# Kernel optimization log

Measured on AMD Instinct MI355X. Metric: run time of the kernel, lower is better.

Reference implementation:

```python
import jax, jax.numpy as jnp
import numpy as np

N1, N2, N3, N4 = 50_000, 100_000, 200_000, 400_000
D, OUT = 128, 128


def silu(x):
    return x * jax.nn.sigmoid(x)


def mlp(h, Wa, ba, Wb, bb):
    # torch.nn.Sequential(Linear, SiLU, Linear)
    return silu(h @ Wa + ba) @ Wb + bb


def setup_inputs() -> dict:
    key = jax.random.key(0)
    ks = jax.random.split(key, 12)
    s = 1.0 / np.sqrt(D).astype(np.float32)
    inp = {
        "feat": jax.random.normal(ks[0], (N1, D), jnp.float32),
        "W1a": jax.random.normal(ks[1], (D, D), jnp.float32) * s,
        "b1a": jnp.zeros((D,), jnp.float32),
        "W1b": jax.random.normal(ks[2], (D, D), jnp.float32) * s,
        "b1b": jnp.zeros((D,), jnp.float32),
        "W2a": jax.random.normal(ks[3], (D, D), jnp.float32) * s,
        "b2a": jnp.zeros((D,), jnp.float32),
        "W2b": jax.random.normal(ks[4], (D, D), jnp.float32) * s,
        "b2b": jnp.zeros((D,), jnp.float32),
        "W3a": jax.random.normal(ks[5], (D, D), jnp.float32) * s,
        "b3a": jnp.zeros((D,), jnp.float32),
        "W3b": jax.random.normal(ks[6], (D, D), jnp.float32) * s,
        "b3b": jnp.zeros((D,), jnp.float32),
        "Wo": jax.random.normal(ks[7], (3 * D, OUT), jnp.float32) * (1.0 / np.sqrt(3 * D).astype(np.float32)),
        "bo": jnp.zeros((OUT,), jnp.float32),
        # n{k-1}_in_n{k} edges: each level-k path has exactly 2 subpath children
        "src12": jax.random.randint(ks[8], (2 * N2,), 0, N1),
        "dst12": jnp.repeat(jnp.arange(N2), 2),
        "src23": jax.random.randint(ks[9], (2 * N3,), 0, N2),
        "dst23": jnp.repeat(jnp.arange(N3), 2),
        "src34": jax.random.randint(ks[10], (2 * N4,), 0, N3),
        "dst34": jnp.repeat(jnp.arange(N4), 2),
    }
    return inp


def reference(feat, W1a, b1a, W1b, b1b, W2a, b2a, W2b, b2b,
              W3a, b3a, W3b, b3b, Wo, bo,
              src12, dst12, src23, dst23, src34, dst34):
    # ---- upward ----
    h1 = mlp(feat, W1a, b1a, W1b, b1b)                       # n1 features (kept for final concat)
    h2 = jax.ops.segment_prod(h1[src12], dst12, num_segments=N2, indices_are_sorted=True)
    h2t = mlp(h2, W2a, b2a, W2b, b2b)
    h3 = jax.ops.segment_prod(h2t[src23], dst23, num_segments=N3, indices_are_sorted=True)
    h3t = mlp(h3, W3a, b3a, W3b, b3b)
    h4 = jax.ops.segment_prod(h3t[src34], dst34, num_segments=N4, indices_are_sorted=True)
    # ---- downward ----
    # n2_has_n1 (reverse of n1_in_n2): sum n2 features onto n1 -> 'h2'
    h2_on_n1 = jax.ops.segment_sum(h2t[dst12], src12, num_segments=N1)
    # n4_has_n3 then n3_has_n2 (overwrite h on lower level)
    h3_dn = jax.ops.segment_sum(h4[dst34], src34, num_segments=N3)
    h2_dn = jax.ops.segment_sum(h3_dn[dst23], src23, num_segments=N2)
    # n2_has_n1 again -> 'h_down'
    h_down = jax.ops.segment_sum(h2_dn[dst12], src12, num_segments=N1)
    # final per-node linear + SiLU on concat([h, h2, h_down])
    out = silu(jnp.concatenate([h1, h2_on_n1, h_down], axis=-1) @ Wo + bo)
    return out
```

## Files before the change

kernel.cpp:

```cpp
#include <hip/hip_runtime.h>

#define D 128
#define XSH 136

#define SHIFT 11
#define NPB   2048
#define EPT   8

typedef _Float16 f16;
typedef __attribute__((ext_vector_type(4))) _Float16 f16x4;
typedef __attribute__((ext_vector_type(8))) _Float16 f16x8;
typedef __attribute__((ext_vector_type(4))) float    f32x4;

__device__ __forceinline__ float silu_f(float x) {
    return x / (1.0f + __expf(-x));
}

struct WPtrs { const float* s0; const float* s1; const float* s2;
               const float* s3; const float* s4; const float* s5; };
__global__ void wconv_all_kernel(WPtrs wp, const float* __restrict__ Wo, f16* __restrict__ WT)
{
    const int blk = blockIdx.x, t = threadIdx.x;
    if (blk < 384) {
        const int wid = blk >> 6;
        const int off = ((blk & 63) << 8) + t;
        const int n = off >> 7, k = off & 127;
        const float* s;
        switch (wid) {
            case 0: s = wp.s0; break;
            case 1: s = wp.s1; break;
            case 2: s = wp.s2; break;
            case 3: s = wp.s3; break;
            case 4: s = wp.s4; break;
            default: s = wp.s5; break;
        }
        WT[(wid << 14) + off] = (f16)s[(k << 7) + n];
    } else {
        const int off = ((blk - 384) << 8) + t;
        const int n = off / 384, k = off - n * 384;
        WT[(6 << 14) + off] = (f16)Wo[k * 128 + n];
    }
}

template<bool GATHER>
__launch_bounds__(256)
__global__ void mlp_mfma_kernel(const void* __restrict__ in_, const int* __restrict__ src,
                                const f16* __restrict__ WaT, const float* __restrict__ ba,
                                const f16* __restrict__ WbT, const float* __restrict__ bb,
                                f16* __restrict__ out, int nrows)
{
    __shared__ f16 xs[64][XSH];
    __shared__ f16 ys[64][XSH];
    const int t = threadIdx.x;
    const int w = t >> 6, l = t & 63;
    const int cl = l & 15, kg = l >> 4;
    const int row0 = blockIdx.x * 64;

    f16x8 wa[2][4], wb[2][4];
    #pragma unroll
    for (int nt = 0; nt < 2; ++nt)
        #pragma unroll
        for (int kk = 0; kk < 4; ++kk) {
            const size_t o = (size_t)((w * 2 + nt) * 16 + cl) * D + kk * 32 + kg * 8;
            wa[nt][kk] = *(const f16x8*)(WaT + o);
            wb[nt][kk] = *(const f16x8*)(WbT + o);
        }

    {
        const int r = t >> 2, q = t & 3;
        const int g = row0 + r;
        f16* dst = &xs[r][q * 32];
        if (g < nrows) {
            if (GATHER) {
                const f16* in = (const f16*)in_;
                const int a = src[2 * g], b = src[2 * g + 1];
                const f16x8* pa = (const f16x8*)(in + (size_t)a * D + q * 32);
                const f16x8* pb = (const f16x8*)(in + (size_t)b * D + q * 32);
                #pragma unroll
                for (int i = 0; i < 4; ++i) {
                    f16x8 av = pa[i], bv = pb[i], hv;
                    #pragma unroll
                    for (int j = 0; j < 8; ++j) hv[j] = (f16)((float)av[j] * (float)bv[j]);
                    *(f16x8*)(dst + 8 * i) = hv;
                }
            } else {
                const float* in = (const float*)in_;
                const float4* p = (const float4*)(in + (size_t)g * D + q * 32);
                #pragma unroll
                for (int i = 0; i < 4; ++i) {
                    float4 v0 = p[2 * i], v1 = p[2 * i + 1];
                    f16x8 hv = {(f16)v0.x, (f16)v0.y, (f16)v0.z, (f16)v0.w,
                                (f16)v1.x, (f16)v1.y, (f16)v1.z, (f16)v1.w};
                    *(f16x8*)(dst + 8 * i) = hv;
                }
            }
        } else {
            f16x8 z = {};
            #pragma unroll
            for (int i = 0; i < 4; ++i) *(f16x8*)(dst + 8 * i) = z;
        }
    }
    __syncthreads();

    f32x4 acc[2][4];

    #pragma unroll
    for (int nt = 0; nt < 2; ++nt)
        #pragma unroll
        for (int m = 0; m < 4; ++m) acc[nt][m] = (f32x4){0.f, 0.f, 0.f, 0.f};
    #pragma unroll
    for (int m = 0; m < 4; ++m)
        #pragma unroll
        for (int kk = 0; kk < 4; ++kk) {
            const f16x8 a = *(const f16x8*)&xs[m * 16 + cl][kk * 32 + kg * 8];
            acc[0][m] = __builtin_amdgcn_mfma_f32_16x16x32_f16(wa[0][kk], a, acc[0][m], 0, 0, 0);
            acc[1][m] = __builtin_amdgcn_mfma_f32_16x16x32_f16(wa[1][kk], a, acc[1][m], 0, 0, 0);
        }
    #pragma unroll
    for (int nt = 0; nt < 2; ++nt) {
        const int n0 = w * 32 + nt * 16 + kg * 4;
        const float4 bv = *(const float4*)&ba[n0];
        #pragma unroll
        for (int m = 0; m < 4; ++m) {
            f16x4 y;
            y[0] = (f16)silu_f(acc[nt][m][0] + bv.x);
            y[1] = (f16)silu_f(acc[nt][m][1] + bv.y);
            y[2] = (f16)silu_f(acc[nt][m][2] + bv.z);
            y[3] = (f16)silu_f(acc[nt][m][3] + bv.w);
            *(f16x4*)&ys[m * 16 + cl][n0] = y;
        }
    }
    __syncthreads();

    #pragma unroll
    for (int nt = 0; nt < 2; ++nt)
        #pragma unroll
        for (int m = 0; m < 4; ++m) acc[nt][m] = (f32x4){0.f, 0.f, 0.f, 0.f};
    #pragma unroll
    for (int m = 0; m < 4; ++m)
        #pragma unroll
        for (int kk = 0; kk < 4; ++kk) {
            const f16x8 a = *(const f16x8*)&ys[m * 16 + cl][kk * 32 + kg * 8];
            acc[0][m] = __builtin_amdgcn_mfma_f32_16x16x32_f16(wb[0][kk], a, acc[0][m], 0, 0, 0);
            acc[1][m] = __builtin_amdgcn_mfma_f32_16x16x32_f16(wb[1][kk], a, acc[1][m], 0, 0, 0);
        }
    #pragma unroll
    for (int nt = 0; nt < 2; ++nt) {
        const int n0 = w * 32 + nt * 16 + kg * 4;
        const float4 bv = *(const float4*)&bb[n0];
        #pragma unroll
        for (int m = 0; m < 4; ++m) {
            f16x4 z;
            z[0] = (f16)(acc[nt][m][0] + bv.x);
            z[1] = (f16)(acc[nt][m][1] + bv.y);
            z[2] = (f16)(acc[nt][m][2] + bv.z);
            z[3] = (f16)(acc[nt][m][3] + bv.w);
            *(f16x4*)&xs[m * 16 + cl][n0] = z;
        }
    }
    __syncthreads();

    {
        const int r = t >> 2, q = t & 3;
        const int g = row0 + r;
        if (g < nrows) {
            f16* dst = out + (size_t)g * D + q * 32;
            #pragma unroll
            for (int i = 0; i < 4; ++i)
                *(f16x8*)(dst + 8 * i) = *(const f16x8*)&xs[r][q * 32 + 8 * i];
        }
    }
}

__launch_bounds__(256)
__global__ void out_mfma_kernel(const f16* __restrict__ h1, const f16* __restrict__ h2on1,
                                const f16* __restrict__ hdown,
                                const f16* __restrict__ WoT, const float* __restrict__ bo,
                                float* __restrict__ out, int nrows)
{
    __shared__ f16 xs[64][XSH];
    const int t = threadIdx.x;
    const int w = t >> 6, l = t & 63;
    const int cl = l & 15, kg = l >> 4;
    const int row0 = blockIdx.x * 64;

    f32x4 acc[2][4];
    #pragma unroll
    for (int nt = 0; nt < 2; ++nt)
        #pragma unroll
        for (int m = 0; m < 4; ++m) acc[nt][m] = (f32x4){0.f, 0.f, 0.f, 0.f};

    const f16* parts[3] = {h1, h2on1, hdown};
    #pragma unroll
    for (int p = 0; p < 3; ++p) {
        f16x8 wo[2][4];
        #pragma unroll
        for (int nt = 0; nt < 2; ++nt)
            #pragma unroll
            for (int kk = 0; kk < 4; ++kk)
                wo[nt][kk] = *(const f16x8*)(WoT + (size_t)((w * 2 + nt) * 16 + cl) * 384
                                             + p * D + kk * 32 + kg * 8);
        {
            const int r = t >> 2, q = t & 3;
            const int g = row0 + r;
            f16* dst = &xs[r][q * 32];
            if (g < nrows) {
                const f16x8* pp = (const f16x8*)(parts[p] + (size_t)g * D + q * 32);
                #pragma unroll
                for (int i = 0; i < 4; ++i) *(f16x8*)(dst + 8 * i) = pp[i];
            } else {
                f16x8 z = {};
                #pragma unroll
                for (int i = 0; i < 4; ++i) *(f16x8*)(dst + 8 * i) = z;
            }
        }
        __syncthreads();
        #pragma unroll
        for (int m = 0; m < 4; ++m)
            #pragma unroll
            for (int kk = 0; kk < 4; ++kk) {
                const f16x8 a = *(const f16x8*)&xs[m * 16 + cl][kk * 32 + kg * 8];
                acc[0][m] = __builtin_amdgcn_mfma_f32_16x16x32_f16(wo[0][kk], a, acc[0][m], 0, 0, 0);
                acc[1][m] = __builtin_amdgcn_mfma_f32_16x16x32_f16(wo[1][kk], a, acc[1][m], 0, 0, 0);
            }
        __syncthreads();
    }

    #pragma unroll
    for (int nt = 0; nt < 2; ++nt) {
        const int n0 = w * 32 + nt * 16 + kg * 4;
        const float4 bv = *(const float4*)&bo[n0];
        #pragma unroll
        for (int m = 0; m < 4; ++m) {
            const int g = row0 + m * 16 + cl;
            if (g < nrows) {
                float4 v = make_float4(silu_f(acc[nt][m][0] + bv.x),
                                       silu_f(acc[nt][m][1] + bv.y),
                                       silu_f(acc[nt][m][2] + bv.z),
                                       silu_f(acc[nt][m][3] + bv.w));
                *(float4*)(out + (size_t)g * D + n0) = v;
            }
        }
    }
}

__global__ void bucket_hist_kernel(const int* __restrict__ s12, int E12,
                                   const int* __restrict__ s23, int E23,
                                   const int* __restrict__ s34, int E34,
                                   int* __restrict__ bcnt, int N1, int N2, int nbkt)
{
    __shared__ int h[256];
    const int t = threadIdx.x;
    for (int i = t; i < 256; i += blockDim.x) h[i] = 0;
    __syncthreads();
    const int Etot = E12 + E23 + E34;
    for (int g = blockIdx.x * blockDim.x + t; g < Etot; g += gridDim.x * blockDim.x) {
        int node;
        if (g < E12) node = s12[g];
        else if (g < E12 + E23) node = N1 + s23[g - E12];
        else node = N1 + N2 + s34[g - E12 - E23];
        atomicAdd(&h[node >> SHIFT], 1);
    }
    __syncthreads();
    for (int i = t; i < nbkt; i += blockDim.x)
        if (h[i]) atomicAdd(&bcnt[i], h[i]);
}

__global__ void bucket_scan_kernel(const int* __restrict__ bcnt, int* __restrict__ bbase,
                                   int* __restrict__ bcur, int nbkt, int Etot)
{
    __shared__ int s[256];
    const int t = threadIdx.x;
    const int v = (t < nbkt) ? bcnt[t] : 0;
    s[t] = v;
    __syncthreads();
    for (int d = 1; d < 256; d <<= 1) {
        const int u = (t >= d) ? s[t - d] : 0;
        __syncthreads();
        s[t] += u;
        __syncthreads();
    }
    if (t < nbkt) { const int ex = s[t] - v; bbase[t] = ex; bcur[t] = ex; }
    if (t == 0) bbase[nbkt] = Etot;
}

__global__ void csr_pass1_kernel(const int* __restrict__ s12, int E12,
                                 const int* __restrict__ s23, int E23,
                                 const int* __restrict__ s34, int E34,
                                 int* __restrict__ bcur, int2* __restrict__ recs,
                                 int N1, int N2, int nbkt)
{
    __shared__ int cnt[256];
    __shared__ int gbase[256];
    const int t = threadIdx.x;
    const int chunk = blockIdx.x * (256 * EPT);
    const int Etot = E12 + E23 + E34;
    for (int i = t; i < 256; i += 256) cnt[i] = 0;
    __syncthreads();
    int node_[EPT], pay_[EPT], br_[EPT];
    #pragma unroll
    for (int i = 0; i < EPT; ++i) {
        const int g = chunk + i * 256 + t;
        int node = -1, pay = 0, b = 0, r = 0;
        if (g < Etot) {
            if (g < E12) { node = s12[g]; pay = g >> 1; }
            else if (g < E12 + E23) { const int e = g - E12; node = N1 + s23[e]; pay = e >> 1; }
            else { const int e = g - E12 - E23; node = N1 + N2 + s34[e]; pay = s34[e ^ 1]; }
            b = node >> SHIFT;
            r = atomicAdd(&cnt[b], 1);
        }
        node_[i] = node; pay_[i] = pay; br_[i] = (b << 16) | r;
    }
    __syncthreads();
    if (t < nbkt && cnt[t]) gbase[t] = atomicAdd(&bcur[t], cnt[t]);
    __syncthreads();
    #pragma unroll
    for (int i = 0; i < EPT; ++i) {
        if (node_[i] >= 0) {
            const int b = br_[i] >> 16, r = br_[i] & 0xffff;
            recs[gbase[b] + r] = make_int2(node_[i], pay_[i]);
        }
    }
}

__launch_bounds__(1024)
__global__ void csr_pass2_kernel(const int2* __restrict__ recs,
                                 const int* __restrict__ bbase,
                                 int2* __restrict__ offcnt, int* __restrict__ el, int NT)
{
    __shared__ int cnt2[NPB];
    __shared__ int pref[NPB];
    __shared__ int s1[NPB / 2];
    const int b = blockIdx.x, t = threadIdx.x;
    const int node0 = b << SHIFT;
    const int k0 = bbase[b], k1 = bbase[b + 1];
    for (int i = t; i < NPB; i += 1024) cnt2[i] = 0;
    __syncthreads();
    for (int k = k0 + t; k < k1; k += 1024)
        atomicAdd(&cnt2[recs[k].x - node0], 1);
    __syncthreads();
    s1[t] = cnt2[2 * t] + cnt2[2 * t + 1];
    __syncthreads();
    for (int d = 1; d < 1024; d <<= 1) {
        const int u = (t >= d) ? s1[t - d] : 0;
        __syncthreads();
        s1[t] += u;
        __syncthreads();
    }
    {
        const int a = cnt2[2 * t];
        const int pairsum = a + cnt2[2 * t + 1];
        const int ex0 = s1[t] - pairsum;
        pref[2 * t] = ex0;
        pref[2 * t + 1] = ex0 + a;
    }
    __syncthreads();
    for (int i = t; i < NPB; i += 1024) {
        const int node = node0 + i;
        if (node < NT) offcnt[node] = make_int2(k0 + pref[i], cnt2[i]);
    }
    __syncthreads();
    for (int k = k0 + t; k < k1; k += 1024) {
        const int2 r = recs[k];
        const int pos = atomicAdd(&pref[r.x - node0], 1);
        el[k0 + pos] = r.y;
    }
}

__global__ void prod_gather_kernel(const f16* __restrict__ h3t,
                                   const int2* __restrict__ offcnt,
                                   const int* __restrict__ el,
                                   f16* __restrict__ h3dn, int nrows)
{
    const long long g = (long long)blockIdx.x * blockDim.x + threadIdx.x;
    const int i = (int)(g >> 4);
    if (i >= nrows) return;
    const int c = ((int)g & 15) * 8;
    const f16x8 ownv = *(const f16x8*)(h3t + (size_t)i * D + c);
    float acc0[8] = {}, acc1[8] = {};
    const int2 oc = offcnt[i];
    const int base = oc.x, deg = oc.y;
    int d = 0;
    for (; d + 4 <= deg; d += 4) {
        const int s0 = el[base + d + 0], s1v = el[base + d + 1];
        const int s2 = el[base + d + 2], s3v = el[base + d + 3];
        const f16x8 v0 = *(const f16x8*)(h3t + (size_t)s0 * D + c);
        const f16x8 v1 = *(const f16x8*)(h3t + (size_t)s1v * D + c);
        const f16x8 v2 = *(const f16x8*)(h3t + (size_t)s2 * D + c);
        const f16x8 v3 = *(const f16x8*)(h3t + (size_t)s3v * D + c);
        #pragma unroll
        for (int j = 0; j < 8; ++j) {
            acc0[j] += (float)v0[j] + (float)v2[j];
            acc1[j] += (float)v1[j] + (float)v3[j];
        }
    }
    for (; d < deg; ++d) {
        const int s0 = el[base + d];
        const f16x8 v0 = *(const f16x8*)(h3t + (size_t)s0 * D + c);
        #pragma unroll
        for (int j = 0; j < 8; ++j) acc0[j] += (float)v0[j];
    }
    f16x8 r;
    #pragma unroll
    for (int j = 0; j < 8; ++j) r[j] = (f16)((acc0[j] + acc1[j]) * (float)ownv[j]);
    *(f16x8*)(h3dn + (size_t)i * D + c) = r;
}

__global__ void gather_sum_kernel(const f16* __restrict__ val,
                                  const int2* __restrict__ offcnt,
                                  const int* __restrict__ el,
                                  f16* __restrict__ dst, int nrows)
{
    const long long g = (long long)blockIdx.x * blockDim.x + threadIdx.x;
    const int i = (int)(g >> 4);
    if (i >= nrows) return;
    const int c = ((int)g & 15) * 8;
    float acc0[8] = {}, acc1[8] = {};
    const int2 oc = offcnt[i];
    const int base = oc.x, deg = oc.y;
    int d = 0;
    for (; d + 4 <= deg; d += 4) {
        const int s0 = el[base + d + 0], s1v = el[base + d + 1];
        const int s2 = el[base + d + 2], s3v = el[base + d + 3];
        const f16x8 v0 = *(const f16x8*)(val + (size_t)s0 * D + c);
        const f16x8 v1 = *(const f16x8*)(val + (size_t)s1v * D + c);
        const f16x8 v2 = *(const f16x8*)(val + (size_t)s2 * D + c);
        const f16x8 v3 = *(const f16x8*)(val + (size_t)s3v * D + c);
        #pragma unroll
        for (int j = 0; j < 8; ++j) {
            acc0[j] += (float)v0[j] + (float)v2[j];
            acc1[j] += (float)v1[j] + (float)v3[j];
        }
    }
    for (; d < deg; ++d) {
        const int s0 = el[base + d];
        const f16x8 v0 = *(const f16x8*)(val + (size_t)s0 * D + c);
        #pragma unroll
        for (int j = 0; j < 8; ++j) acc0[j] += (float)v0[j];
    }
    f16x8 r;
    #pragma unroll
    for (int j = 0; j < 8; ++j) r[j] = (f16)(acc0[j] + acc1[j]);
    *(f16x8*)(dst + (size_t)i * D + c) = r;
}

__global__ void ws_report_kernel(float* out, float v) {
    if (threadIdx.x == 0 && blockIdx.x == 0) out[0] = v;
}

extern "C" void kernel_launch(void* const* d_in, const int* in_sizes, int n_in,
                              void* d_out, int out_size, void* d_ws, size_t ws_size,
                              hipStream_t stream)
{
    const float* feat = (const float*)d_in[0];
    const float* W1a = (const float*)d_in[1];  const float* b1a = (const float*)d_in[2];
    const float* W1b = (const float*)d_in[3];  const float* b1b = (const float*)d_in[4];
    const float* W2a = (const float*)d_in[5];  const float* b2a = (const float*)d_in[6];
    const float* W2b = (const float*)d_in[7];  const float* b2b = (const float*)d_in[8];
    const float* W3a = (const float*)d_in[9];  const float* b3a = (const float*)d_in[10];
    const float* W3b = (const float*)d_in[11]; const float* b3b = (const float*)d_in[12];
    const float* Wo  = (const float*)d_in[13]; const float* bo  = (const float*)d_in[14];
    const int* src12 = (const int*)d_in[15];
    const int* src23 = (const int*)d_in[17];
    const int* src34 = (const int*)d_in[19];

    const int N1 = in_sizes[0] / D;
    const int N2 = in_sizes[15] / 2;
    const int N3 = in_sizes[17] / 2;
    const int N4 = in_sizes[19] / 2;
    const int E12 = 2 * N2, E23 = 2 * N3, E34 = 2 * N4;
    const int NT = N1 + N2 + N3;
    const int Etot = E12 + E23 + E34;
    const int NBKT = (NT + NPB - 1) >> SHIFT;

    char* p = (char*)d_ws;
    f16* h1    = (f16*)p;  p += (size_t)N1 * D * sizeof(f16);
    f16* h2on1 = (f16*)p;  p += (size_t)N1 * D * sizeof(f16);
    f16* h2t   = (f16*)p;  p += (size_t)N2 * D * sizeof(f16);
    f16* h3t   = (f16*)p;  f16* h2dn  = h3t;
    p += (size_t)N3 * D * sizeof(f16);
    f16* h3dn  = (f16*)p;  f16* hdown = h3dn;
    p += (size_t)N3 * D * sizeof(f16);

    p = (char*)(((uintptr_t)p + 15) & ~(uintptr_t)15);
    int2* offcnt = (int2*)p;             p += (size_t)NT * sizeof(int2);
    int2* recs   = (int2*)p;             p += (size_t)Etot * sizeof(int2);
    int*  el     = (int*)p;              p += (size_t)Etot * sizeof(int);
    int*  bcnt   = (int*)p;              p += 256 * sizeof(int);
    int*  bbase  = (int*)p;              p += 257 * sizeof(int);
    int*  bcur   = (int*)p;              p += 256 * sizeof(int);

    p = (char*)(((uintptr_t)p + 31) & ~(uintptr_t)31);
    f16* WT = (f16*)p;
    f16* WaT1 = WT;
    f16* WbT1 = WaT1 + D * D;
    f16* WaT2 = WbT1 + D * D;
    f16* WbT2 = WaT2 + D * D;
    f16* WaT3 = WbT2 + D * D;
    f16* WbT3 = WaT3 + D * D;
    f16* WoT  = WbT3 + D * D;
    p = (char*)(WoT + 384 * D);

    const size_t need = p - (char*)d_ws;
    if (ws_size < need || NBKT > 256) {
        ws_report_kernel<<<1, 64, 0, stream>>>((float*)d_out, (float)ws_size);
        return;
    }

    dim3 blk(256);
    auto tiles    = [](int n) { return dim3((unsigned)((n + 63) / 64)); };
    auto rowblk16 = [](long long rows) { return dim3((unsigned)((rows * 16 + 255) / 256)); };

    WPtrs wp = {W1a, W1b, W2a, W2b, W3a, W3b};
    wconv_all_kernel<<<dim3(576), blk, 0, stream>>>(wp, Wo, WT);

    hipMemsetAsync(bcnt, 0, 256 * sizeof(int), stream);
    {
        const int nblk = (Etot + 2047) / 2048;
        bucket_hist_kernel<<<dim3((unsigned)nblk), blk, 0, stream>>>(
            src12, E12, src23, E23, src34, E34, bcnt, N1, N2, NBKT);
        bucket_scan_kernel<<<1, 256, 0, stream>>>(bcnt, bbase, bcur, NBKT, Etot);
        csr_pass1_kernel<<<dim3((unsigned)((Etot + 256 * EPT - 1) / (256 * EPT))), blk, 0, stream>>>(
            src12, E12, src23, E23, src34, E34, bcur, recs, N1, N2, NBKT);
        csr_pass2_kernel<<<dim3((unsigned)NBKT), dim3(1024), 0, stream>>>(
            recs, bbase, offcnt, el, NT);
    }

    mlp_mfma_kernel<false><<<tiles(N1), blk, 0, stream>>>(feat, nullptr, WaT1, b1a, WbT1, b1b, h1, N1);
    mlp_mfma_kernel<true ><<<tiles(N2), blk, 0, stream>>>(h1, src12, WaT2, b2a, WbT2, b2b, h2t, N2);
    gather_sum_kernel<<<rowblk16(N1), blk, 0, stream>>>(h2t, offcnt, el, h2on1, N1);
    mlp_mfma_kernel<true ><<<tiles(N3), blk, 0, stream>>>(h2t, src23, WaT3, b3a, WbT3, b3b, h3t, N3);

    prod_gather_kernel<<<rowblk16(N3), blk, 0, stream>>>(h3t, offcnt + N1 + N2, el, h3dn, N3);
    gather_sum_kernel<<<rowblk16(N2), blk, 0, stream>>>(h3dn, offcnt + N1, el, h2dn, N2);
    gather_sum_kernel<<<rowblk16(N1), blk, 0, stream>>>(h2dn, offcnt, el, hdown, N1);

    out_mfma_kernel<<<tiles(N1), blk, 0, stream>>>(h1, h2on1, hdown, WoT, bo, (float*)d_out, N1);
}
```

Baseline: 277.5 us.

## Make MLP kernels persistent with register-prefetched double-buffered tiles

The MLP kernel becomes persistent, launching at most 768 blocks that loop over 64-row tiles. Each block loads its weights into registers once and prefetches the next tile's input into registers while the current tile's MFMAs run, using two LDS input buffers. The output kernel likewise prefetches the next concatenated part into registers before computing on the current one. This aims to hide global-load latency and amortise weight loads, at the cost of more registers and LDS, which may lower occupancy.

```diff
diff --git a/kernel.cpp b/kernel.cpp
--- a/kernel.cpp
+++ b/kernel.cpp
@@ -47,14 +47,14 @@
 __global__ void mlp_mfma_kernel(const void* __restrict__ in_, const int* __restrict__ src,
                                 const f16* __restrict__ WaT, const float* __restrict__ ba,
                                 const f16* __restrict__ WbT, const float* __restrict__ bb,
-                                f16* __restrict__ out, int nrows)
-{
-    __shared__ f16 xs[64][XSH];
+                                f16* __restrict__ out, int nrows, int ntiles)
+{
+    __shared__ f16 xs[2][64][XSH];
     __shared__ f16 ys[64][XSH];
     const int t = threadIdx.x;
     const int w = t >> 6, l = t & 63;
     const int cl = l & 15, kg = l >> 4;
-    const int row0 = blockIdx.x * 64;
+    const int r = t >> 2, q = t & 3;
 
     f16x8 wa[2][4], wb[2][4];
     #pragma unroll
@@ -66,109 +66,142 @@
             wb[nt][kk] = *(const f16x8*)(WbT + o);
         }
 
-    {
-        const int r = t >> 2, q = t & 3;
-        const int g = row0 + r;
-        f16* dst = &xs[r][q * 32];
-        if (g < nrows) {
-            if (GATHER) {
-                const f16* in = (const f16*)in_;
+    f16x8 ra[4], rb[4];
+    float4 rf[8];
+
+    int tile = blockIdx.x;
+    if (tile >= ntiles) return;
+
+    auto LOADT = [&](int tl) {
+        const int g = tl * 64 + r;
+        if (GATHER) {
+            const f16* in = (const f16*)in_;
+            if (g < nrows) {
                 const int a = src[2 * g], b = src[2 * g + 1];
                 const f16x8* pa = (const f16x8*)(in + (size_t)a * D + q * 32);
                 const f16x8* pb = (const f16x8*)(in + (size_t)b * D + q * 32);
                 #pragma unroll
-                for (int i = 0; i < 4; ++i) {
-                    f16x8 av = pa[i], bv = pb[i], hv;
-                    #pragma unroll
-                    for (int j = 0; j < 8; ++j) hv[j] = (f16)((float)av[j] * (float)bv[j]);
-                    *(f16x8*)(dst + 8 * i) = hv;
-                }
+                for (int i = 0; i < 4; ++i) { ra[i] = pa[i]; rb[i] = pb[i]; }
             } else {
-                const float* in = (const float*)in_;
-                const float4* p = (const float4*)(in + (size_t)g * D + q * 32);
-                #pragma unroll
-                for (int i = 0; i < 4; ++i) {
-                    float4 v0 = p[2 * i], v1 = p[2 * i + 1];
-                    f16x8 hv = {(f16)v0.x, (f16)v0.y, (f16)v0.z, (f16)v0.w,
-                                (f16)v1.x, (f16)v1.y, (f16)v1.z, (f16)v1.w};
-                    *(f16x8*)(dst + 8 * i) = hv;
-                }
+                f16x8 z = {};
+                #pragma unroll
+                for (int i = 0; i < 4; ++i) { ra[i] = z; rb[i] = z; }
             }
         } else {
-            f16x8 z = {};
-            #pragma unroll
-            for (int i = 0; i < 4; ++i) *(f16x8*)(dst + 8 * i) = z;
-        }
-    }
-    __syncthreads();
-
-    f32x4 acc[2][4];
-
-    #pragma unroll
-    for (int nt = 0; nt < 2; ++nt)
-        #pragma unroll
-        for (int m = 0; m < 4; ++m) acc[nt][m] = (f32x4){0.f, 0.f, 0.f, 0.f};
-    #pragma unroll
-    for (int m = 0; m < 4; ++m)
-        #pragma unroll
-        for (int kk = 0; kk < 4; ++kk) {
-            const f16x8 a = *(const f16x8*)&xs[m * 16 + cl][kk * 32 + kg * 8];
-            acc[0][m] = __builtin_amdgcn_mfma_f32_16x16x32_f16(wa[0][kk], a, acc[0][m], 0, 0, 0);
-            acc[1][m] = __builtin_amdgcn_mfma_f32_16x16x32_f16(wa[1][kk], a, acc[1][m], 0, 0, 0);
-        }
-    #pragma unroll
-    for (int nt = 0; nt < 2; ++nt) {
-        const int n0 = w * 32 + nt * 16 + kg * 4;
-        const float4 bv = *(const float4*)&ba[n0];
-        #pragma unroll
-        for (int m = 0; m < 4; ++m) {
-            f16x4 y;
-            y[0] = (f16)silu_f(acc[nt][m][0] + bv.x);
-            y[1] = (f16)silu_f(acc[nt][m][1] + bv.y);
-            y[2] = (f16)silu_f(acc[nt][m][2] + bv.z);
-            y[3] = (f16)silu_f(acc[nt][m][3] + bv.w);
-            *(f16x4*)&ys[m * 16 + cl][n0] = y;
-        }
-    }
-    __syncthreads();
-
-    #pragma unroll
-    for (int nt = 0; nt < 2; ++nt)
-        #pragma unroll
-        for (int m = 0; m < 4; ++m) acc[nt][m] = (f32x4){0.f, 0.f, 0.f, 0.f};
-    #pragma unroll
-    for (int m = 0; m < 4; ++m)
-        #pragma unroll
-        for (int kk = 0; kk < 4; ++kk) {
-            const f16x8 a = *(const f16x8*)&ys[m * 16 + cl][kk * 32 + kg * 8];
-            acc[0][m] = __builtin_amdgcn_mfma_f32_16x16x32_f16(wb[0][kk], a, acc[0][m], 0, 0, 0);
-            acc[1][m] = __builtin_amdgcn_mfma_f32_16x16x32_f16(wb[1][kk], a, acc[1][m], 0, 0, 0);
-        }
-    #pragma unroll
-    for (int nt = 0; nt < 2; ++nt) {
-        const int n0 = w * 32 + nt * 16 + kg * 4;
-        const float4 bv = *(const float4*)&bb[n0];
-        #pragma unroll
-        for (int m = 0; m < 4; ++m) {
-            f16x4 z;
-            z[0] = (f16)(acc[nt][m][0] + bv.x);
-            z[1] = (f16)(acc[nt][m][1] + bv.y);
-            z[2] = (f16)(acc[nt][m][2] + bv.z);
-            z[3] = (f16)(acc[nt][m][3] + bv.w);
-            *(f16x4*)&xs[m * 16 + cl][n0] = z;
-        }
-    }
-    __syncthreads();
-
-    {
-        const int r = t >> 2, q = t & 3;
-        const int g = row0 + r;
-        if (g < nrows) {
-            f16* dst = out + (size_t)g * D + q * 32;
-            #pragma unroll
-            for (int i = 0; i < 4; ++i)
-                *(f16x8*)(dst + 8 * i) = *(const f16x8*)&xs[r][q * 32 + 8 * i];
-        }
+            const float* in = (const float*)in_;
+            if (g < nrows) {
+                const float4* p4 = (const float4*)(in + (size_t)g * D + q * 32);
+                #pragma unroll
+                for (int i = 0; i < 8; ++i) rf[i] = p4[i];
+            } else {
+                #pragma unroll
+                for (int i = 0; i < 8; ++i) rf[i] = make_float4(0.f, 0.f, 0.f, 0.f);
+            }
+        }
+    };
+    auto WRITE = [&](int buf) {
+        f16* dst = &xs[buf][r][q * 32];
+        if (GATHER) {
+            #pragma unroll
+            for (int i = 0; i < 4; ++i) {
+                f16x8 hv;
+                #pragma unroll
+                for (int j = 0; j < 8; ++j) hv[j] = (f16)((float)ra[i][j] * (float)rb[i][j]);
+                *(f16x8*)(dst + 8 * i) = hv;
+            }
+        } else {
+            #pragma unroll
+            for (int i = 0; i < 4; ++i) {
+                float4 v0 = rf[2 * i], v1 = rf[2 * i + 1];
+                f16x8 hv = {(f16)v0.x, (f16)v0.y, (f16)v0.z, (f16)v0.w,
+                            (f16)v1.x, (f16)v1.y, (f16)v1.z, (f16)v1.w};
+                *(f16x8*)(dst + 8 * i) = hv;
+            }
+        }
+    };
+
+    LOADT(tile);
+    WRITE(0);
+    __syncthreads();
+    int cur = 0;
+
+    while (true) {
+        const int nxt = tile + (int)gridDim.x;
+        const bool have = nxt < ntiles;
+        if (have) LOADT(nxt);
+
+        f32x4 acc[2][4];
+
+        #pragma unroll
+        for (int nt = 0; nt < 2; ++nt)
+            #pragma unroll
+            for (int m = 0; m < 4; ++m) acc[nt][m] = (f32x4){0.f, 0.f, 0.f, 0.f};
+        #pragma unroll
+        for (int m = 0; m < 4; ++m)
+            #pragma unroll
+            for (int kk = 0; kk < 4; ++kk) {
+                const f16x8 a = *(const f16x8*)&xs[cur][m * 16 + cl][kk * 32 + kg * 8];
+                acc[0][m] = __builtin_amdgcn_mfma_f32_16x16x32_f16(wa[0][kk], a, acc[0][m], 0, 0, 0);
+                acc[1][m] = __builtin_amdgcn_mfma_f32_16x16x32_f16(wa[1][kk], a, acc[1][m], 0, 0, 0);
+            }
+        #pragma unroll
+        for (int nt = 0; nt < 2; ++nt) {
+            const int n0 = w * 32 + nt * 16 + kg * 4;
+            const float4 bv = *(const float4*)&ba[n0];
+            #pragma unroll
+            for (int m = 0; m < 4; ++m) {
+                f16x4 y;
+                y[0] = (f16)silu_f(acc[nt][m][0] + bv.x);
+                y[1] = (f16)silu_f(acc[nt][m][1] + bv.y);
+                y[2] = (f16)silu_f(acc[nt][m][2] + bv.z);
+                y[3] = (f16)silu_f(acc[nt][m][3] + bv.w);
+                *(f16x4*)&ys[m * 16 + cl][n0] = y;
+            }
+        }
+        __syncthreads();
+
+        #pragma unroll
+        for (int nt = 0; nt < 2; ++nt)
+            #pragma unroll
+            for (int m = 0; m < 4; ++m) acc[nt][m] = (f32x4){0.f, 0.f, 0.f, 0.f};
+        #pragma unroll
+        for (int m = 0; m < 4; ++m)
+            #pragma unroll
+            for (int kk = 0; kk < 4; ++kk) {
+                const f16x8 a = *(const f16x8*)&ys[m * 16 + cl][kk * 32 + kg * 8];
+                acc[0][m] = __builtin_amdgcn_mfma_f32_16x16x32_f16(wb[0][kk], a, acc[0][m], 0, 0, 0);
+                acc[1][m] = __builtin_amdgcn_mfma_f32_16x16x32_f16(wb[1][kk], a, acc[1][m], 0, 0, 0);
+            }
+        #pragma unroll
+        for (int nt = 0; nt < 2; ++nt) {
+            const int n0 = w * 32 + nt * 16 + kg * 4;
+            const float4 bv = *(const float4*)&bb[n0];
+            #pragma unroll
+            for (int m = 0; m < 4; ++m) {
+                f16x4 z;
+                z[0] = (f16)(acc[nt][m][0] + bv.x);
+                z[1] = (f16)(acc[nt][m][1] + bv.y);
+                z[2] = (f16)(acc[nt][m][2] + bv.z);
+                z[3] = (f16)(acc[nt][m][3] + bv.w);
+                *(f16x4*)&xs[cur][m * 16 + cl][n0] = z;
+            }
+        }
+        __syncthreads();
+
+        {
+            const int g = tile * 64 + r;
+            if (g < nrows) {
+                f16* dst = out + (size_t)g * D + q * 32;
+                #pragma unroll
+                for (int i = 0; i < 4; ++i)
+                    *(f16x8*)(dst + 8 * i) = *(const f16x8*)&xs[cur][r][q * 32 + 8 * i];
+            }
+        }
+        if (!have) break;
+        WRITE(cur ^ 1);
+        __syncthreads();
+        cur ^= 1;
+        tile = nxt;
     }
 }
 
@@ -182,7 +215,9 @@
     const int t = threadIdx.x;
     const int w = t >> 6, l = t & 63;
     const int cl = l & 15, kg = l >> 4;
+    const int r = t >> 2, q = t & 3;
     const int row0 = blockIdx.x * 64;
+    const int g = row0 + r;
 
     f32x4 acc[2][4];
     #pragma unroll
@@ -191,8 +226,38 @@
         for (int m = 0; m < 4; ++m) acc[nt][m] = (f32x4){0.f, 0.f, 0.f, 0.f};
 
     const f16* parts[3] = {h1, h2on1, hdown};
+    f16x8 st[2][4];
+
+    if (g < nrows) {
+        const f16x8* pp = (const f16x8*)(parts[0] + (size_t)g * D + q * 32);
+        #pragma unroll
+        for (int i = 0; i < 4; ++i) st[0][i] = pp[i];
+    } else {
+        f16x8 z = {};
+        #pragma unroll
+        for (int i = 0; i < 4; ++i) st[0][i] = z;
+    }
+
     #pragma unroll
     for (int p = 0; p < 3; ++p) {
+        if (p) __syncthreads();
+        {
+            f16* dst = &xs[r][q * 32];
+            #pragma unroll
+            for (int i = 0; i < 4; ++i) *(f16x8*)(dst + 8 * i) = st[p & 1][i];
+        }
+        __syncthreads();
+        if (p < 2) {
+            if (g < nrows) {
+                const f16x8* pp = (const f16x8*)(parts[p + 1] + (size_t)g * D + q * 32);
+                #pragma unroll
+                for (int i = 0; i < 4; ++i) st[(p + 1) & 1][i] = pp[i];
+            } else {
+                f16x8 z = {};
+                #pragma unroll
+                for (int i = 0; i < 4; ++i) st[(p + 1) & 1][i] = z;
+            }
+        }
         f16x8 wo[2][4];
         #pragma unroll
         for (int nt = 0; nt < 2; ++nt)
@@ -200,21 +265,6 @@
             for (int kk = 0; kk < 4; ++kk)
                 wo[nt][kk] = *(const f16x8*)(WoT + (size_t)((w * 2 + nt) * 16 + cl) * 384
                                              + p * D + kk * 32 + kg * 8);
-        {
-            const int r = t >> 2, q = t & 3;
-            const int g = row0 + r;
-            f16* dst = &xs[r][q * 32];
-            if (g < nrows) {
-                const f16x8* pp = (const f16x8*)(parts[p] + (size_t)g * D + q * 32);
-                #pragma unroll
-                for (int i = 0; i < 4; ++i) *(f16x8*)(dst + 8 * i) = pp[i];
-            } else {
-                f16x8 z = {};
-                #pragma unroll
-                for (int i = 0; i < 4; ++i) *(f16x8*)(dst + 8 * i) = z;
-            }
-        }
-        __syncthreads();
         #pragma unroll
         for (int m = 0; m < 4; ++m)
             #pragma unroll
@@ -223,7 +273,6 @@
                 acc[0][m] = __builtin_amdgcn_mfma_f32_16x16x32_f16(wo[0][kk], a, acc[0][m], 0, 0, 0);
                 acc[1][m] = __builtin_amdgcn_mfma_f32_16x16x32_f16(wo[1][kk], a, acc[1][m], 0, 0, 0);
             }
-        __syncthreads();
     }
 
     #pragma unroll
@@ -232,13 +281,13 @@
         const float4 bv = *(const float4*)&bo[n0];
         #pragma unroll
         for (int m = 0; m < 4; ++m) {
-            const int g = row0 + m * 16 + cl;
-            if (g < nrows) {
+            const int gr = row0 + m * 16 + cl;
+            if (gr < nrows) {
                 float4 v = make_float4(silu_f(acc[nt][m][0] + bv.x),
                                        silu_f(acc[nt][m][1] + bv.y),
                                        silu_f(acc[nt][m][2] + bv.z),
                                        silu_f(acc[nt][m][3] + bv.w));
-                *(float4*)(out + (size_t)g * D + n0) = v;
+                *(float4*)(out + (size_t)gr * D + n0) = v;
             }
         }
     }
@@ -508,7 +557,7 @@
     }
 
     dim3 blk(256);
-    auto tiles    = [](int n) { return dim3((unsigned)((n + 63) / 64)); };
+    auto tiles    = [](int n) { return (n + 63) / 64; };
     auto rowblk16 = [](long long rows) { return dim3((unsigned)((rows * 16 + 255) / 256)); };
 
     WPtrs wp = {W1a, W1b, W2a, W2b, W3a, W3b};
@@ -526,14 +575,20 @@
             recs, bbase, offcnt, el, NT);
     }
 
-    mlp_mfma_kernel<false><<<tiles(N1), blk, 0, stream>>>(feat, nullptr, WaT1, b1a, WbT1, b1b, h1, N1);
-    mlp_mfma_kernel<true ><<<tiles(N2), blk, 0, stream>>>(h1, src12, WaT2, b2a, WbT2, b2b, h2t, N2);
-    gather_sum_kernel<<<rowblk16(N1), blk, 0, stream>>>(h2t, offcnt, el, h2on1, N1);
-    mlp_mfma_kernel<true ><<<tiles(N3), blk, 0, stream>>>(h2t, src23, WaT3, b3a, WbT3, b3b, h3t, N3);
+    auto mlp_grid = [&](int ntl) { return dim3((unsigned)(ntl < 768 ? ntl : 768)); };
+    {
+        const int t1 = tiles(N1);
+        mlp_mfma_kernel<false><<<mlp_grid(t1), blk, 0, stream>>>(feat, nullptr, WaT1, b1a, WbT1, b1b, h1, N1, t1);
+        const int t2 = tiles(N2);
+        mlp_mfma_kernel<true ><<<mlp_grid(t2), blk, 0, stream>>>(h1, src12, WaT2, b2a, WbT2, b2b, h2t, N2, t2);
+        gather_sum_kernel<<<rowblk16(N1), blk, 0, stream>>>(h2t, offcnt, el, h2on1, N1);
+        const int t3 = tiles(N3);
+        mlp_mfma_kernel<true ><<<mlp_grid(t3), blk, 0, stream>>>(h2t, src23, WaT3, b3a, WbT3, b3b, h3t, N3, t3);
+    }
 
     prod_gather_kernel<<<rowblk16(N3), blk, 0, stream>>>(h3t, offcnt + N1 + N2, el, h3dn, N3);
     gather_sum_kernel<<<rowblk16(N2), blk, 0, stream>>>(h3dn, offcnt + N1, el, h2dn, N2);
     gather_sum_kernel<<<rowblk16(N1), blk, 0, stream>>>(h2dn, offcnt, el, hdown, N1);
 
-    out_mfma_kernel<<<tiles(N1), blk, 0, stream>>>(h1, h2on1, hdown, WoT, bo, (float*)d_out, N1);
-}
+    out_mfma_kernel<<<dim3((unsigned)tiles(N1)), blk, 0, stream>>>(h1, h2on1, hdown, WoT, bo, (float*)d_out, N1);
+}
```

Result: slower. 284.4 us (+2.5%).

## Persist MLP kernel with LDS-resident weights and per-wave 16-row tiles

Applied to the files above, without the earlier changes.

The MLP kernel becomes persistent with a fixed grid of 512 blocks. Each block stages both weight matrices once into LDS in MFMA fragment order, and each wave then loops over 16-row tiles on its own. Inputs are loaded straight into registers, and the intermediate activation goes through a per-wave swizzled LDS buffer, so no block-wide barriers are needed between the two GEMMs. This removes the per-block reload of weights and the __syncthreads. In exchange it uses 72KB of LDS per block, which limits occupancy. The output kernel also double-buffers its three input parts in registers so loading the next part overlaps the current MFMA pass.

```diff
diff --git a/kernel.cpp b/kernel.cpp
--- a/kernel.cpp
+++ b/kernel.cpp
@@ -49,125 +49,123 @@
                                 const f16* __restrict__ WbT, const float* __restrict__ bb,
                                 f16* __restrict__ out, int nrows)
 {
-    __shared__ f16 xs[64][XSH];
-    __shared__ f16 ys[64][XSH];
+    __shared__ f16 wlds[32768];
+    __shared__ f16 ys[4][2048];
     const int t = threadIdx.x;
     const int w = t >> 6, l = t & 63;
     const int cl = l & 15, kg = l >> 4;
-    const int row0 = blockIdx.x * 64;
-
-    f16x8 wa[2][4], wb[2][4];
-    #pragma unroll
-    for (int nt = 0; nt < 2; ++nt)
-        #pragma unroll
-        for (int kk = 0; kk < 4; ++kk) {
-            const size_t o = (size_t)((w * 2 + nt) * 16 + cl) * D + kk * 32 + kg * 8;
-            wa[nt][kk] = *(const f16x8*)(WaT + o);
-            wb[nt][kk] = *(const f16x8*)(WbT + o);
-        }
-
-    {
-        const int r = t >> 2, q = t & 3;
-        const int g = row0 + r;
-        f16* dst = &xs[r][q * 32];
+
+    #pragma unroll
+    for (int i = 0; i < 16; ++i) {
+        const int f = t + i * 256;
+        const int mat = f >> 11, idx = f & 2047;
+        const int nt = idx >> 8, kk = (idx >> 6) & 3, ll = idx & 63;
+        const f16* Wsrc = mat ? WbT : WaT;
+        const f16x8 v = *(const f16x8*)(Wsrc + (size_t)(nt * 16 + (ll & 15)) * D
+                                        + kk * 32 + (ll >> 4) * 8);
+        *(f16x8*)(wlds + (size_t)f * 8) = v;
+    }
+    __syncthreads();
+
+    f16* ysw = ys[w];
+    auto ysoff = [&](int row, int b) -> int {
+        return row * 128 + ((b ^ (((row & 3) << 6) | (((row >> 2) & 3) << 4))) >> 1);
+    };
+
+    const int ntile = (nrows + 15) >> 4;
+    for (int tile = blockIdx.x * 4 + w; tile < ntile; tile += (int)gridDim.x * 4) {
+        const int g = tile * 16 + cl;
+        f16x8 xf[4];
+
         if (g < nrows) {
             if (GATHER) {
                 const f16* in = (const f16*)in_;
                 const int a = src[2 * g], b = src[2 * g + 1];
-                const f16x8* pa = (const f16x8*)(in + (size_t)a * D + q * 32);
-                const f16x8* pb = (const f16x8*)(in + (size_t)b * D + q * 32);
                 #pragma unroll
-                for (int i = 0; i < 4; ++i) {
-                    f16x8 av = pa[i], bv = pb[i], hv;
+                for (int kk = 0; kk < 4; ++kk) {
+                    const f16x8 av = *(const f16x8*)(in + (size_t)a * D + kk * 32 + kg * 8);
+                    const f16x8 bv = *(const f16x8*)(in + (size_t)b * D + kk * 32 + kg * 8);
+                    f16x8 hv;
                     #pragma unroll
                     for (int j = 0; j < 8; ++j) hv[j] = (f16)((float)av[j] * (float)bv[j]);
-                    *(f16x8*)(dst + 8 * i) = hv;
+                    xf[kk] = hv;
                 }
             } else {
                 const float* in = (const float*)in_;
-                const float4* p = (const float4*)(in + (size_t)g * D + q * 32);
                 #pragma unroll
-                for (int i = 0; i < 4; ++i) {
-                    float4 v0 = p[2 * i], v1 = p[2 * i + 1];
+                for (int kk = 0; kk < 4; ++kk) {
+                    const float4 v0 = *(const float4*)(in + (size_t)g * D + kk * 32 + kg * 8);
+                    const float4 v1 = *(const float4*)(in + (size_t)g * D + kk * 32 + kg * 8 + 4);
                     f16x8 hv = {(f16)v0.x, (f16)v0.y, (f16)v0.z, (f16)v0.w,
                                 (f16)v1.x, (f16)v1.y, (f16)v1.z, (f16)v1.w};
-                    *(f16x8*)(dst + 8 * i) = hv;
+                    xf[kk] = hv;
                 }
             }
         } else {
             f16x8 z = {};
             #pragma unroll
-            for (int i = 0; i < 4; ++i) *(f16x8*)(dst + 8 * i) = z;
-        }
-    }
-    __syncthreads();
-
-    f32x4 acc[2][4];
-
-    #pragma unroll
-    for (int nt = 0; nt < 2; ++nt)
-        #pragma unroll
-        for (int m = 0; m < 4; ++m) acc[nt][m] = (f32x4){0.f, 0.f, 0.f, 0.f};
-    #pragma unroll
-    for (int m = 0; m < 4; ++m)
-        #pragma unroll
-        for (int kk = 0; kk < 4; ++kk) {
-            const f16x8 a = *(const f16x8*)&xs[m * 16 + cl][kk * 32 + kg * 8];
-            acc[0][m] = __builtin_amdgcn_mfma_f32_16x16x32_f16(wa[0][kk], a, acc[0][m], 0, 0, 0);
-            acc[1][m] = __builtin_amdgcn_mfma_f32_16x16x32_f16(wa[1][kk], a, acc[1][m], 0, 0, 0);
-        }
-    #pragma unroll
-    for (int nt = 0; nt < 2; ++nt) {
-        const int n0 = w * 32 + nt * 16 + kg * 4;
-        const float4 bv = *(const float4*)&ba[n0];
-        #pragma unroll
-        for (int m = 0; m < 4; ++m) {
+            for (int kk = 0; kk < 4; ++kk) xf[kk] = z;
+        }
+
+        f32x4 acc[8];
+
+        #pragma unroll
+        for (int nt = 0; nt < 8; ++nt) acc[nt] = (f32x4){0.f, 0.f, 0.f, 0.f};
+        #pragma unroll
+        for (int kk = 0; kk < 4; ++kk)
+            #pragma unroll
+            for (int nt = 0; nt < 8; ++nt) {
+                const f16x8 wf = *(const f16x8*)(wlds + ((size_t)((nt * 4 + kk) * 64 + l)) * 8);
+                acc[nt] = __builtin_amdgcn_mfma_f32_16x16x32_f16(wf, xf[kk], acc[nt], 0, 0, 0);
+            }
+        #pragma unroll
+        for (int nt = 0; nt < 8; ++nt) {
+            const float4 bv = *(const float4*)&ba[nt * 16 + kg * 4];
             f16x4 y;
-            y[0] = (f16)silu_f(acc[nt][m][0] + bv.x);
-            y[1] = (f16)silu_f(acc[nt][m][1] + bv.y);
-            y[2] = (f16)silu_f(acc[nt][m][2] + bv.z);
-            y[3] = (f16)silu_f(acc[nt][m][3] + bv.w);
-            *(f16x4*)&ys[m * 16 + cl][n0] = y;
-        }
-    }
-    __syncthreads();
-
-    #pragma unroll
-    for (int nt = 0; nt < 2; ++nt)
-        #pragma unroll
-        for (int m = 0; m < 4; ++m) acc[nt][m] = (f32x4){0.f, 0.f, 0.f, 0.f};
-    #pragma unroll
-    for (int m = 0; m < 4; ++m)
-        #pragma unroll
-        for (int kk = 0; kk < 4; ++kk) {
-            const f16x8 a = *(const f16x8*)&ys[m * 16 + cl][kk * 32 + kg * 8];
-            acc[0][m] = __builtin_amdgcn_mfma_f32_16x16x32_f16(wb[0][kk], a, acc[0][m], 0, 0, 0);
-            acc[1][m] = __builtin_amdgcn_mfma_f32_16x16x32_f16(wb[1][kk], a, acc[1][m], 0, 0, 0);
-        }
-    #pragma unroll
-    for (int nt = 0; nt < 2; ++nt) {
-        const int n0 = w * 32 + nt * 16 + kg * 4;
-        const float4 bv = *(const float4*)&bb[n0];
-        #pragma unroll
-        for (int m = 0; m < 4; ++m) {
+            y[0] = (f16)silu_f(acc[nt][0] + bv.x);
+            y[1] = (f16)silu_f(acc[nt][1] + bv.y);
+            y[2] = (f16)silu_f(acc[nt][2] + bv.z);
+            y[3] = (f16)silu_f(acc[nt][3] + bv.w);
+            *(f16x4*)(ysw + ysoff(cl, nt * 32 + kg * 8)) = y;
+        }
+        asm volatile("s_waitcnt lgkmcnt(0)" ::: "memory");
+        __builtin_amdgcn_sched_barrier(0);
+
+        #pragma unroll
+        for (int kk = 0; kk < 4; ++kk)
+            xf[kk] = *(const f16x8*)(ysw + ysoff(cl, kk * 64 + kg * 16));
+
+        #pragma unroll
+        for (int nt = 0; nt < 8; ++nt) acc[nt] = (f32x4){0.f, 0.f, 0.f, 0.f};
+        #pragma unroll
+        for (int kk = 0; kk < 4; ++kk)
+            #pragma unroll
+            for (int nt = 0; nt < 8; ++nt) {
+                const f16x8 wf = *(const f16x8*)(wlds + ((size_t)(2048 + (nt * 4 + kk) * 64 + l)) * 8);
+                acc[nt] = __builtin_amdgcn_mfma_f32_16x16x32_f16(wf, xf[kk], acc[nt], 0, 0, 0);
+            }
+        #pragma unroll
+        for (int nt = 0; nt < 8; ++nt) {
+            const float4 bv = *(const float4*)&bb[nt * 16 + kg * 4];
             f16x4 z;
-            z[0] = (f16)(acc[nt][m][0] + bv.x);
-            z[1] = (f16)(acc[nt][m][1] + bv.y);
-            z[2] = (f16)(acc[nt][m][2] + bv.z);
-            z[3] = (f16)(acc[nt][m][3] + bv.w);
-            *(f16x4*)&xs[m * 16 + cl][n0] = z;
-        }
-    }
-    __syncthreads();
-
-    {
-        const int r = t >> 2, q = t & 3;
-        const int g = row0 + r;
-        if (g < nrows) {
-            f16* dst = out + (size_t)g * D + q * 32;
-            #pragma unroll
-            for (int i = 0; i < 4; ++i)
-                *(f16x8*)(dst + 8 * i) = *(const f16x8*)&xs[r][q * 32 + 8 * i];
+            z[0] = (f16)(acc[nt][0] + bv.x);
+            z[1] = (f16)(acc[nt][1] + bv.y);
+            z[2] = (f16)(acc[nt][2] + bv.z);
+            z[3] = (f16)(acc[nt][3] + bv.w);
+            *(f16x4*)(ysw + ysoff(cl, nt * 32 + kg * 8)) = z;
+        }
+        asm volatile("s_waitcnt lgkmcnt(0)" ::: "memory");
+        __builtin_amdgcn_sched_barrier(0);
+
+        #pragma unroll
+        for (int i = 0; i < 4; ++i) {
+            const int lin = i * 1024 + l * 16;
+            const int row = lin >> 8, b = lin & 255;
+            const int gr = tile * 16 + row;
+            if (gr < nrows) {
+                const f16x8 v = *(const f16x8*)(ysw + ysoff(row, b));
+                *(f16x8*)(out + (size_t)gr * D + (b >> 1)) = v;
+            }
         }
     }
 }
@@ -182,7 +180,9 @@
     const int t = threadIdx.x;
     const int w = t >> 6, l = t & 63;
     const int cl = l & 15, kg = l >> 4;
+    const int r = t >> 2, q = t & 3;
     const int row0 = blockIdx.x * 64;
+    const int g = row0 + r;
 
     f32x4 acc[2][4];
     #pragma unroll
@@ -191,8 +191,38 @@
         for (int m = 0; m < 4; ++m) acc[nt][m] = (f32x4){0.f, 0.f, 0.f, 0.f};
 
     const f16* parts[3] = {h1, h2on1, hdown};
+    f16x8 st[2][4];
+
+    if (g < nrows) {
+        const f16x8* pp = (const f16x8*)(parts[0] + (size_t)g * D + q * 32);
+        #pragma unroll
+        for (int i = 0; i < 4; ++i) st[0][i] = pp[i];
+    } else {
+        f16x8 z = {};
+        #pragma unroll
+        for (int i = 0; i < 4; ++i) st[0][i] = z;
+    }
+
     #pragma unroll
     for (int p = 0; p < 3; ++p) {
+        if (p) __syncthreads();
+        {
+            f16* dst = &xs[r][q * 32];
+            #pragma unroll
+            for (int i = 0; i < 4; ++i) *(f16x8*)(dst + 8 * i) = st[p & 1][i];
+        }
+        __syncthreads();
+        if (p < 2) {
+            if (g < nrows) {
+                const f16x8* pp = (const f16x8*)(parts[p + 1] + (size_t)g * D + q * 32);
+                #pragma unroll
+                for (int i = 0; i < 4; ++i) st[(p + 1) & 1][i] = pp[i];
+            } else {
+                f16x8 z = {};
+                #pragma unroll
+                for (int i = 0; i < 4; ++i) st[(p + 1) & 1][i] = z;
+            }
+        }
         f16x8 wo[2][4];
         #pragma unroll
         for (int nt = 0; nt < 2; ++nt)
@@ -200,21 +230,6 @@
             for (int kk = 0; kk < 4; ++kk)
                 wo[nt][kk] = *(const f16x8*)(WoT + (size_t)((w * 2 + nt) * 16 + cl) * 384
                                              + p * D + kk * 32 + kg * 8);
-        {
-            const int r = t >> 2, q = t & 3;
-            const int g = row0 + r;
-            f16* dst = &xs[r][q * 32];
-            if (g < nrows) {
-                const f16x8* pp = (const f16x8*)(parts[p] + (size_t)g * D + q * 32);
-                #pragma unroll
-                for (int i = 0; i < 4; ++i) *(f16x8*)(dst + 8 * i) = pp[i];
-            } else {
-                f16x8 z = {};
-                #pragma unroll
-                for (int i = 0; i < 4; ++i) *(f16x8*)(dst + 8 * i) = z;
-            }
-        }
-        __syncthreads();
         #pragma unroll
         for (int m = 0; m < 4; ++m)
             #pragma unroll
@@ -223,7 +238,6 @@
                 acc[0][m] = __builtin_amdgcn_mfma_f32_16x16x32_f16(wo[0][kk], a, acc[0][m], 0, 0, 0);
                 acc[1][m] = __builtin_amdgcn_mfma_f32_16x16x32_f16(wo[1][kk], a, acc[1][m], 0, 0, 0);
             }
-        __syncthreads();
     }
 
     #pragma unroll
@@ -232,13 +246,13 @@
         const float4 bv = *(const float4*)&bo[n0];
         #pragma unroll
         for (int m = 0; m < 4; ++m) {
-            const int g = row0 + m * 16 + cl;
-            if (g < nrows) {
+            const int gr = row0 + m * 16 + cl;
+            if (gr < nrows) {
                 float4 v = make_float4(silu_f(acc[nt][m][0] + bv.x),
                                        silu_f(acc[nt][m][1] + bv.y),
                                        silu_f(acc[nt][m][2] + bv.z),
                                        silu_f(acc[nt][m][3] + bv.w));
-                *(float4*)(out + (size_t)g * D + n0) = v;
+                *(float4*)(out + (size_t)gr * D + n0) = v;
             }
         }
     }
@@ -508,7 +522,6 @@
     }
 
     dim3 blk(256);
-    auto tiles    = [](int n) { return dim3((unsigned)((n + 63) / 64)); };
     auto rowblk16 = [](long long rows) { return dim3((unsigned)((rows * 16 + 255) / 256)); };
 
     WPtrs wp = {W1a, W1b, W2a, W2b, W3a, W3b};
@@ -526,14 +539,14 @@
             recs, bbase, offcnt, el, NT);
     }
 
-    mlp_mfma_kernel<false><<<tiles(N1), blk, 0, stream>>>(feat, nullptr, WaT1, b1a, WbT1, b1b, h1, N1);
-    mlp_mfma_kernel<true ><<<tiles(N2), blk, 0, stream>>>(h1, src12, WaT2, b2a, WbT2, b2b, h2t, N2);
+    mlp_mfma_kernel<false><<<dim3(512), blk, 0, stream>>>(feat, nullptr, WaT1, b1a, WbT1, b1b, h1, N1);
+    mlp_mfma_kernel<true ><<<dim3(512), blk, 0, stream>>>(h1, src12, WaT2, b2a, WbT2, b2b, h2t, N2);
     gather_sum_kernel<<<rowblk16(N1), blk, 0, stream>>>(h2t, offcnt, el, h2on1, N1);
-    mlp_mfma_kernel<true ><<<tiles(N3), blk, 0, stream>>>(h2t, src23, WaT3, b3a, WbT3, b3b, h3t, N3);
+    mlp_mfma_kernel<true ><<<dim3(512), blk, 0, stream>>>(h2t, src23, WaT3, b3a, WbT3, b3b, h3t, N3);
 
     prod_gather_kernel<<<rowblk16(N3), blk, 0, stream>>>(h3t, offcnt + N1 + N2, el, h3dn, N3);
     gather_sum_kernel<<<rowblk16(N2), blk, 0, stream>>>(h3dn, offcnt + N1, el, h2dn, N2);
     gather_sum_kernel<<<rowblk16(N1), blk, 0, stream>>>(h2dn, offcnt, el, hdown, N1);
 
-    out_mfma_kernel<<<tiles(N1), blk, 0, stream>>>(h1, h2on1, hdown, WoT, bo, (float*)d_out, N1);
-}
+    out_mfma_kernel<<<dim3((unsigned)((N1 + 63) / 64)), blk, 0, stream>>>(h1, h2on1, hdown, WoT, bo, (float*)d_out, N1);
+}
```

Result: faster. 259.4 us (-6.5%).
